# Kernel tuning notes

Hardware: AMD Instinct MI355X
Metric: run time of the kernel (lower is better)

The kernel has to match this reference:

```python
import jax, jax.numpy as jnp
import numpy as np


def setup_inputs() -> dict:
    key = jax.random.key(0)
    ks = jax.random.split(key, 8)
    B, N, A, H = 2, 2048, 256, 8
    KD = A // H  # key_dim per head = 32
    VD = A // H  # value_dim per head = 32
    return {
        "q_data": jax.random.normal(ks[0], (B, N, A), dtype=jnp.float32),
        "bias": jax.random.normal(ks[1], (B, N), dtype=jnp.float32),
        "nonbatched_bias": jax.random.normal(ks[2], (H, N, N), dtype=jnp.float32),
        "query_w": jax.random.normal(ks[3], (A, H, KD), dtype=jnp.float32) * 0.05,
        "query_b": jax.random.normal(ks[4], (1, H, KD), dtype=jnp.float32) * 0.05,
        "key_w": jax.random.normal(ks[5], (A, H, KD), dtype=jnp.float32) * 0.05,
        "value_w": jax.random.normal(ks[6], (A, H, VD), dtype=jnp.float32) * 0.05,
        "gating_w": jax.random.normal(ks[7], (A, H, VD), dtype=jnp.float32) * 0.05,
    }


def reference(q_data, bias, nonbatched_bias, query_w, query_b, key_w, value_w, gating_w):
    # q_data: [b, n, a]; bias: [b, n_k]; nonbatched_bias: [h, n_q, n_k]
    key_dim = query_w.shape[-1]
    scale = key_dim ** (-0.5)
    # projections (fused QKV in the original kernel)
    q = (jnp.einsum("bqa,ahc->bqhc", q_data, query_w) + query_b) * scale  # [b,q,h,c]
    k = jnp.einsum("bka,ahc->bkhc", q_data, key_w)                        # [b,k,h,c]
    v = jnp.einsum("bka,ahv->bkhv", q_data, value_w)                      # [b,k,h,v]
    # attention logits + batched bias (over keys) + shared nonbatched bias
    logits = jnp.einsum("bqhc,bkhc->bhqk", q, k)
    logits = logits + bias[:, None, None, :] + nonbatched_bias[None]
    weights = jax.nn.softmax(logits, axis=-1)                             # [b,h,q,k]
    weighted = jnp.einsum("bhqk,bkhv->bqhv", weights, v)                  # [b,q,h,v]
    # sigmoid gating branch fused after value projection
    gate = jax.nn.sigmoid(jnp.einsum("bqa,ahv->bqhv", q_data, gating_w))
    return weighted * gate                                                # [b,q,h,v]
```

## Files before the change

kernel.cpp:

```cpp
#include <hip/hip_runtime.h>
#include <stdint.h>

#define NTOK 2048
#define SCALE 0.17677669529663687f

typedef short s16x8 __attribute__((ext_vector_type(8)));
typedef unsigned short u16x8 __attribute__((ext_vector_type(8)));
typedef float f32x4 __attribute__((ext_vector_type(4)));

__device__ __forceinline__ unsigned short f2bf(float f) {
  unsigned int u = __builtin_bit_cast(unsigned int, f);
  u += 0x7fffu + ((u >> 16) & 1u);
  return (unsigned short)(u >> 16);
}

__global__ __launch_bounds__(256) void prep_weights_k(
    const float* __restrict__ qw, const float* __restrict__ kw,
    const float* __restrict__ vw, const float* __restrict__ gw,
    unsigned short* __restrict__ Wt) {
  __shared__ float tile[64][68];
  const int p = blockIdx.z;
  const int a0 = blockIdx.x * 64;
  const int n0 = blockIdx.y * 64;
  const float* src = (p == 0) ? qw : (p == 1) ? kw : (p == 2) ? vw : gw;
  const int tx = threadIdx.x & 15;
  const int ty = threadIdx.x >> 4;
#pragma unroll
  for (int kk = 0; kk < 4; kk++) {
    int ar = ty + kk * 16;
    float4 v = *reinterpret_cast<const float4*>(src + (a0 + ar) * 256 + n0 + tx * 4);
    tile[ar][tx * 4 + 0] = v.x; tile[ar][tx * 4 + 1] = v.y;
    tile[ar][tx * 4 + 2] = v.z; tile[ar][tx * 4 + 3] = v.w;
  }
  __syncthreads();
  unsigned short* dst = Wt + p * 65536;
#pragma unroll
  for (int kk = 0; kk < 4; kk++) {
    int nr = ty + kk * 16;
    ushort4 o;
    o.x = f2bf(tile[tx * 4 + 0][nr]);
    o.y = f2bf(tile[tx * 4 + 1][nr]);
    o.z = f2bf(tile[tx * 4 + 2][nr]);
    o.w = f2bf(tile[tx * 4 + 3][nr]);
    *reinterpret_cast<ushort4*>(dst + (n0 + nr) * 256 + a0 + tx * 4) = o;
  }
}

__global__ __launch_bounds__(256) void proj_k(
    const float* __restrict__ x, const unsigned short* __restrict__ Wt,
    const float* __restrict__ query_b,
    unsigned short* __restrict__ Qg, unsigned short* __restrict__ Kg,
    unsigned short* __restrict__ Vt, float* __restrict__ gate) {
  const int w = threadIdx.x >> 6;
  const int lane = threadIdx.x & 63;
  const int l15 = lane & 15;
  const int quad = lane >> 4;
  const int p = blockIdx.y >> 1;
  const int half = blockIdx.y & 1;
  const int rbase = blockIdx.x * 128 + w * 32;
  const unsigned short* wp = Wt + p * 65536;

  f32x4 acc[2][8];
#pragma unroll
  for (int rt = 0; rt < 2; rt++)
#pragma unroll
    for (int ct = 0; ct < 8; ct++) acc[rt][ct] = (f32x4){0.f, 0.f, 0.f, 0.f};

  for (int ks = 0; ks < 8; ks++) {
    const int kb = ks * 32;
    s16x8 af[2];
#pragma unroll
    for (int rt = 0; rt < 2; rt++) {
      const float* xr = x + (rbase + rt * 16 + l15) * 256 + kb + quad * 8;
      float4 f0 = *reinterpret_cast<const float4*>(xr);
      float4 f1 = *reinterpret_cast<const float4*>(xr + 4);
      u16x8 t;
      t[0] = f2bf(f0.x); t[1] = f2bf(f0.y); t[2] = f2bf(f0.z); t[3] = f2bf(f0.w);
      t[4] = f2bf(f1.x); t[5] = f2bf(f1.y); t[6] = f2bf(f1.z); t[7] = f2bf(f1.w);
      af[rt] = __builtin_bit_cast(s16x8, t);
    }
#pragma unroll
    for (int ct = 0; ct < 8; ct++) {
      uint4 bv = *reinterpret_cast<const uint4*>(
          wp + (half * 128 + ct * 16 + l15) * 256 + kb + quad * 8);
      s16x8 bfr = __builtin_bit_cast(s16x8, bv);
#pragma unroll
      for (int rt = 0; rt < 2; rt++)
        acc[rt][ct] = __builtin_amdgcn_mfma_f32_16x16x32_bf16(af[rt], bfr, acc[rt][ct], 0, 0, 0);
    }
  }

#pragma unroll
  for (int ct = 0; ct < 8; ct++) {
    const int cgl = half * 128 + ct * 16 + l15;
    const int h = cgl >> 5, c = cgl & 31;
#pragma unroll
    for (int rt = 0; rt < 2; rt++) {
      const int n0r = rbase + rt * 16 + quad * 4;
      const int bidx = n0r >> 11;
      const int nl0 = n0r & 2047;
      if (p == 0) {
        const float qb = query_b[cgl];
#pragma unroll
        for (int i = 0; i < 4; i++) {
          float v = (acc[rt][ct][i] + qb) * SCALE;
          Qg[(size_t)((bidx * 8 + h) * 2048 + nl0 + i) * 32 + c] = f2bf(v);
        }
      } else if (p == 1) {
#pragma unroll
        for (int i = 0; i < 4; i++)
          Kg[(size_t)((bidx * 8 + h) * 2048 + nl0 + i) * 32 + c] = f2bf(acc[rt][ct][i]);
      } else if (p == 2) {
        ushort4 o;
        o.x = f2bf(acc[rt][ct][0]); o.y = f2bf(acc[rt][ct][1]);
        o.z = f2bf(acc[rt][ct][2]); o.w = f2bf(acc[rt][ct][3]);
        *reinterpret_cast<ushort4*>(Vt + (size_t)((bidx * 8 + h) * 32 + c) * 2048 + nl0) = o;
      } else {
#pragma unroll
        for (int i = 0; i < 4; i++) {
          float s = 1.f / (1.f + __expf(-acc[rt][ct][i]));
          gate[(size_t)(bidx * 2048 + nl0 + i) * 256 + cgl] = s;
        }
      }
    }
  }
}

#define PST 136
__global__ __launch_bounds__(128, 2) void attn_k(
    const unsigned short* __restrict__ Qg, const unsigned short* __restrict__ Kg,
    const unsigned short* __restrict__ Vt, const float* __restrict__ bias,
    const float* __restrict__ nb, const float* __restrict__ gate,
    float* __restrict__ out) {
  __shared__ unsigned short Ps[2 * 16 * PST];
  const int w = threadIdx.x >> 6;
  const int lane = threadIdx.x & 63;
  const int l15 = lane & 15;
  const int quad = lane >> 4;
  const int h = blockIdx.y, b = blockIdx.z;
  const int bh = b * 8 + h;
  const int qbase = blockIdx.x * 32 + w * 16;
  const unsigned short* Qp = Qg + (size_t)bh * 2048 * 32;
  const unsigned short* Kp = Kg + (size_t)bh * 2048 * 32;
  const unsigned short* Vp = Vt + (size_t)bh * 32 * 2048;
  const float* nbp = nb + (size_t)h * 2048 * 2048;
  const float* biasp = bias + b * 2048;
  unsigned short* Pw = Ps + w * 16 * PST;

  s16x8 aq = __builtin_bit_cast(s16x8, *reinterpret_cast<const uint4*>(
      Qp + (size_t)(qbase + l15) * 32 + quad * 8));
  const int qr0 = qbase + quad * 4;

  float mst[4], lst[4];
  f32x4 o[2];
#pragma unroll
  for (int i = 0; i < 4; i++) { mst[i] = -INFINITY; lst[i] = 0.f; }
#pragma unroll
  for (int vt = 0; vt < 2; vt++) o[vt] = (f32x4){0.f, 0.f, 0.f, 0.f};

  float nbuf[2][32];
  float bb[2][8];
#pragma unroll
  for (int ct = 0; ct < 8; ct++) {
    bb[0][ct] = biasp[ct * 16 + l15];
#pragma unroll
    for (int i = 0; i < 4; i++)
      nbuf[0][ct * 4 + i] = nbp[(size_t)(qr0 + i) * 2048 + ct * 16 + l15];
  }

#pragma unroll 2
  for (int kt = 0; kt < 16; kt++) {
    const int kb = kt * 128;
    const int cur = kt & 1, nxt = cur ^ 1;

    s16x8 bk[8];
#pragma unroll
    for (int ct = 0; ct < 8; ct++)
      bk[ct] = __builtin_bit_cast(s16x8, *reinterpret_cast<const uint4*>(
          Kp + (size_t)(kb + ct * 16 + l15) * 32 + quad * 8));

    if (kt < 15) {
      const int kb2 = kb + 128;
#pragma unroll
      for (int ct = 0; ct < 8; ct++) {
        bb[nxt][ct] = biasp[kb2 + ct * 16 + l15];
#pragma unroll
        for (int i = 0; i < 4; i++)
          nbuf[nxt][ct * 4 + i] = nbp[(size_t)(qr0 + i) * 2048 + kb2 + ct * 16 + l15];
      }
    }

    f32x4 s[8];
#pragma unroll
    for (int ct = 0; ct < 8; ct++)
      s[ct] = __builtin_amdgcn_mfma_f32_16x16x32_bf16(
          aq, bk[ct], (f32x4){0.f, 0.f, 0.f, 0.f}, 0, 0, 0);

    s16x8 vbf[4][2];
#pragma unroll
    for (int kc = 0; kc < 4; kc++)
#pragma unroll
      for (int vt = 0; vt < 2; vt++)
        vbf[kc][vt] = __builtin_bit_cast(s16x8, *reinterpret_cast<const uint4*>(
            Vp + (size_t)(vt * 16 + l15) * 2048 + kb + kc * 32 + quad * 8));

#pragma unroll
    for (int ct = 0; ct < 8; ct++)
#pragma unroll
      for (int i = 0; i < 4; i++) s[ct][i] += bb[cur][ct] + nbuf[cur][ct * 4 + i];

    float alpha[4];
#pragma unroll
    for (int i = 0; i < 4; i++) {
      float mx = s[0][i];
#pragma unroll
      for (int ct = 1; ct < 8; ct++) mx = fmaxf(mx, s[ct][i]);
      mx = fmaxf(mx, __shfl_xor(mx, 1));
      mx = fmaxf(mx, __shfl_xor(mx, 2));
      mx = fmaxf(mx, __shfl_xor(mx, 4));
      mx = fmaxf(mx, __shfl_xor(mx, 8));
      float mn = fmaxf(mst[i], mx);
      alpha[i] = __expf(mst[i] - mn);
      mst[i] = mn;
      float sum = 0.f;
#pragma unroll
      for (int ct = 0; ct < 8; ct++) {
        float pv = __expf(s[ct][i] - mn);
        Pw[(quad * 4 + i) * PST + ct * 16 + l15] = f2bf(pv);
        sum += pv;
      }
      sum += __shfl_xor(sum, 1);
      sum += __shfl_xor(sum, 2);
      sum += __shfl_xor(sum, 4);
      sum += __shfl_xor(sum, 8);
      lst[i] = lst[i] * alpha[i] + sum;
    }
#pragma unroll
    for (int vt = 0; vt < 2; vt++)
#pragma unroll
      for (int i = 0; i < 4; i++) o[vt][i] *= alpha[i];

#pragma unroll
    for (int kc = 0; kc < 4; kc++) {
      s16x8 ap = __builtin_bit_cast(s16x8, *reinterpret_cast<const uint4*>(
          &Pw[l15 * PST + kc * 32 + quad * 8]));
#pragma unroll
      for (int vt = 0; vt < 2; vt++)
        o[vt] = __builtin_amdgcn_mfma_f32_16x16x32_bf16(ap, vbf[kc][vt], o[vt], 0, 0, 0);
    }
  }

#pragma unroll
  for (int vt = 0; vt < 2; vt++)
#pragma unroll
    for (int i = 0; i < 4; i++) {
      const int q = qr0 + i;
      const int v = vt * 16 + l15;
      const size_t oidx = (size_t)(b * 2048 + q) * 256 + h * 32 + v;
      out[oidx] = (o[vt][i] / lst[i]) * gate[oidx];
    }
}

extern "C" void kernel_launch(void* const* d_in, const int* in_sizes, int n_in,
                              void* d_out, int out_size, void* d_ws, size_t ws_size,
                              hipStream_t stream) {
  const float* q_data = (const float*)d_in[0];
  const float* bias = (const float*)d_in[1];
  const float* nbb = (const float*)d_in[2];
  const float* qw = (const float*)d_in[3];
  const float* qb = (const float*)d_in[4];
  const float* kw = (const float*)d_in[5];
  const float* vw = (const float*)d_in[6];
  const float* gw = (const float*)d_in[7];
  float* out = (float*)d_out;

  char* ws = (char*)d_ws;
  unsigned short* Wt = (unsigned short*)(ws + 0);
  unsigned short* Qg = (unsigned short*)(ws + 524288);
  unsigned short* Kg = (unsigned short*)(ws + 2621440);
  unsigned short* Vt = (unsigned short*)(ws + 4718592);
  float* gate = (float*)(ws + 6815744);

  prep_weights_k<<<dim3(4, 4, 4), 256, 0, stream>>>(qw, kw, vw, gw, Wt);
  proj_k<<<dim3(32, 8), 256, 0, stream>>>(q_data, Wt, qb, Qg, Kg, Vt, gate);
  attn_k<<<dim3(64, 8, 2), 128, 0, stream>>>(Qg, Kg, Vt, bias, nbb, gate, out);
}
```

Before: 258.0 us.

## Share nonbatched bias tile across both batches via async global-to-LDS loads

The attention kernel now covers both batch elements in one 256-thread block, so the nonbatched bias tile (which depends only on head, not batch) is read from global memory once and shared through LDS. The tile is double-buffered with asynchronous global_load_lds transfers, using an XOR swizzle to avoid bank conflicts, and a block barrier is added each iteration. This halves global traffic for the largest input but adds LDS reads, a per-iteration __syncthreads, and coupling between batch waves.

```diff
diff --git a/kernel.cpp b/kernel.cpp
--- a/kernel.cpp
+++ b/kernel.cpp
@@ -12,6 +12,12 @@
   unsigned int u = __builtin_bit_cast(unsigned int, f);
   u += 0x7fffu + ((u >> 16) & 1u);
   return (unsigned short)(u >> 16);
+}
+
+__device__ __forceinline__ void gld_lds16(const float* g, float* l) {
+  __builtin_amdgcn_global_load_lds(
+      (const __attribute__((address_space(1))) unsigned int*)g,
+      (__attribute__((address_space(3))) unsigned int*)l, 16, 0, 0);
 }
 
 __global__ __launch_bounds__(256) void prep_weights_k(
@@ -127,25 +133,41 @@
 }
 
 #define PST 136
-__global__ __launch_bounds__(128, 2) void attn_k(
+__global__ __launch_bounds__(256, 2) void attn_k(
     const unsigned short* __restrict__ Qg, const unsigned short* __restrict__ Kg,
     const unsigned short* __restrict__ Vt, const float* __restrict__ bias,
     const float* __restrict__ nb, const float* __restrict__ gate,
     float* __restrict__ out) {
-  __shared__ unsigned short Ps[2 * 16 * PST];
+  __shared__ float NbS[2][32 * 128];
+  __shared__ unsigned short Ps[4 * 16 * PST];
   const int w = threadIdx.x >> 6;
   const int lane = threadIdx.x & 63;
   const int l15 = lane & 15;
   const int quad = lane >> 4;
-  const int h = blockIdx.y, b = blockIdx.z;
+  const int qsub = w >> 1;
+  const int b = w & 1;
+  const int h = blockIdx.y;
   const int bh = b * 8 + h;
-  const int qbase = blockIdx.x * 32 + w * 16;
+  const int qtile = blockIdx.x * 32;
+  const int qbase = qtile + qsub * 16;
   const unsigned short* Qp = Qg + (size_t)bh * 2048 * 32;
   const unsigned short* Kp = Kg + (size_t)bh * 2048 * 32;
   const unsigned short* Vp = Vt + (size_t)bh * 32 * 2048;
-  const float* nbp = nb + (size_t)h * 2048 * 2048;
   const float* biasp = bias + b * 2048;
   unsigned short* Pw = Ps + w * 16 * PST;
+
+  const float* nbt = nb + (size_t)h * 2048 * 2048 + (size_t)qtile * 2048;
+  const float* nbl[4];
+  {
+    const int rsub = lane >> 5;
+    const int cblk = lane & 31;
+#pragma unroll
+    for (int j = 0; j < 4; j++) {
+      const int r = w * 8 + j * 2 + rsub;
+      const int c = (cblk ^ (r & 7)) * 4;
+      nbl[j] = nbt + (size_t)r * 2048 + c;
+    }
+  }
 
   s16x8 aq = __builtin_bit_cast(s16x8, *reinterpret_cast<const uint4*>(
       Qp + (size_t)(qbase + l15) * 32 + quad * 8));
@@ -158,15 +180,13 @@
 #pragma unroll
   for (int vt = 0; vt < 2; vt++) o[vt] = (f32x4){0.f, 0.f, 0.f, 0.f};
 
-  float nbuf[2][32];
   float bb[2][8];
 #pragma unroll
-  for (int ct = 0; ct < 8; ct++) {
-    bb[0][ct] = biasp[ct * 16 + l15];
-#pragma unroll
-    for (int i = 0; i < 4; i++)
-      nbuf[0][ct * 4 + i] = nbp[(size_t)(qr0 + i) * 2048 + ct * 16 + l15];
-  }
+  for (int ct = 0; ct < 8; ct++) bb[0][ct] = biasp[ct * 16 + l15];
+
+#pragma unroll
+  for (int j = 0; j < 4; j++) gld_lds16(nbl[j], &NbS[0][(w * 8 + j * 2) * 128]);
+  __syncthreads();
 
 #pragma unroll 2
   for (int kt = 0; kt < 16; kt++) {
@@ -179,15 +199,23 @@
       bk[ct] = __builtin_bit_cast(s16x8, *reinterpret_cast<const uint4*>(
           Kp + (size_t)(kb + ct * 16 + l15) * 32 + quad * 8));
 
+    s16x8 vbf[4][2];
+#pragma unroll
+    for (int kc = 0; kc < 4; kc++)
+#pragma unroll
+      for (int vt = 0; vt < 2; vt++)
+        vbf[kc][vt] = __builtin_bit_cast(s16x8, *reinterpret_cast<const uint4*>(
+            Vp + (size_t)(vt * 16 + l15) * 2048 + kb + kc * 32 + quad * 8));
+
     if (kt < 15) {
       const int kb2 = kb + 128;
 #pragma unroll
-      for (int ct = 0; ct < 8; ct++) {
-        bb[nxt][ct] = biasp[kb2 + ct * 16 + l15];
-#pragma unroll
-        for (int i = 0; i < 4; i++)
-          nbuf[nxt][ct * 4 + i] = nbp[(size_t)(qr0 + i) * 2048 + kb2 + ct * 16 + l15];
-      }
+      for (int ct = 0; ct < 8; ct++) bb[nxt][ct] = biasp[kb2 + ct * 16 + l15];
+      __builtin_amdgcn_sched_barrier(0);
+#pragma unroll
+      for (int j = 0; j < 4; j++)
+        gld_lds16(nbl[j] + kb2, &NbS[nxt][(w * 8 + j * 2) * 128]);
+      __builtin_amdgcn_sched_barrier(0);
     }
 
     f32x4 s[8];
@@ -196,18 +224,16 @@
       s[ct] = __builtin_amdgcn_mfma_f32_16x16x32_bf16(
           aq, bk[ct], (f32x4){0.f, 0.f, 0.f, 0.f}, 0, 0, 0);
 
-    s16x8 vbf[4][2];
-#pragma unroll
-    for (int kc = 0; kc < 4; kc++)
-#pragma unroll
-      for (int vt = 0; vt < 2; vt++)
-        vbf[kc][vt] = __builtin_bit_cast(s16x8, *reinterpret_cast<const uint4*>(
-            Vp + (size_t)(vt * 16 + l15) * 2048 + kb + kc * 32 + quad * 8));
-
-#pragma unroll
-    for (int ct = 0; ct < 8; ct++)
-#pragma unroll
-      for (int i = 0; i < 4; i++) s[ct][i] += bb[cur][ct] + nbuf[cur][ct * 4 + i];
+#pragma unroll
+    for (int i = 0; i < 4; i++) {
+      const int rsw = (quad * 4 + i) & 7;
+      const int rbase = (qsub * 16 + quad * 4 + i) * 128;
+#pragma unroll
+      for (int ct = 0; ct < 8; ct++) {
+        const int col = ct * 16 + l15;
+        s[ct][i] += bb[cur][ct] + NbS[cur][rbase + (col ^ (rsw * 4))];
+      }
+    }
 
     float alpha[4];
 #pragma unroll
@@ -248,6 +274,8 @@
       for (int vt = 0; vt < 2; vt++)
         o[vt] = __builtin_amdgcn_mfma_f32_16x16x32_bf16(ap, vbf[kc][vt], o[vt], 0, 0, 0);
     }
+
+    __syncthreads();
   }
 
 #pragma unroll
@@ -283,5 +311,5 @@
 
   prep_weights_k<<<dim3(4, 4, 4), 256, 0, stream>>>(qw, kw, vw, gw, Wt);
   proj_k<<<dim3(32, 8), 256, 0, stream>>>(q_data, Wt, qb, Qg, Kg, Vt, gate);
-  attn_k<<<dim3(64, 8, 2), 128, 0, stream>>>(Qg, Kg, Vt, bias, nbb, gate, out);
-}
+  attn_k<<<dim3(64, 8), 256, 0, stream>>>(Qg, Kg, Vt, bias, nbb, gate, out);
+}
```

After: 258.3 us. No clear change (+0.1%).

## Split attention key range across two blocks and merge partials in combine kernel

Applied to the files above, without the earlier changes.

Splits the key dimension of the attention kernel into two halves, each handled by its own block, which doubles the grid so more blocks are in flight. Each block writes unnormalized partial outputs plus running max and sum, and a new combine kernel merges the two halves with log-sum-exp rescaling and applies the gate. It also raises the occupancy hint in launch bounds, moves the V loads earlier, and fences the bias prefetch with scheduling barriers. The cost is an extra kernel launch and an extra round trip of partial results through global memory.

```diff
diff --git a/kernel.cpp b/kernel.cpp
--- a/kernel.cpp
+++ b/kernel.cpp
@@ -127,19 +127,22 @@
 }
 
 #define PST 136
-__global__ __launch_bounds__(128, 2) void attn_k(
+__global__ __launch_bounds__(128, 4) void attn_k(
     const unsigned short* __restrict__ Qg, const unsigned short* __restrict__ Kg,
     const unsigned short* __restrict__ Vt, const float* __restrict__ bias,
-    const float* __restrict__ nb, const float* __restrict__ gate,
-    float* __restrict__ out) {
+    const float* __restrict__ nb,
+    float* __restrict__ po, float* __restrict__ pm, float* __restrict__ pl) {
   __shared__ unsigned short Ps[2 * 16 * PST];
   const int w = threadIdx.x >> 6;
   const int lane = threadIdx.x & 63;
   const int l15 = lane & 15;
   const int quad = lane >> 4;
-  const int h = blockIdx.y, b = blockIdx.z;
+  const int h = blockIdx.y;
+  const int b = blockIdx.z >> 1;
+  const int sp = blockIdx.z & 1;
   const int bh = b * 8 + h;
   const int qbase = blockIdx.x * 32 + w * 16;
+  const int kt0 = sp * 8;
   const unsigned short* Qp = Qg + (size_t)bh * 2048 * 32;
   const unsigned short* Kp = Kg + (size_t)bh * 2048 * 32;
   const unsigned short* Vp = Vt + (size_t)bh * 32 * 2048;
@@ -162,14 +165,14 @@
   float bb[2][8];
 #pragma unroll
   for (int ct = 0; ct < 8; ct++) {
-    bb[0][ct] = biasp[ct * 16 + l15];
+    bb[0][ct] = biasp[kt0 * 128 + ct * 16 + l15];
 #pragma unroll
     for (int i = 0; i < 4; i++)
-      nbuf[0][ct * 4 + i] = nbp[(size_t)(qr0 + i) * 2048 + ct * 16 + l15];
+      nbuf[0][ct * 4 + i] = nbp[(size_t)(qr0 + i) * 2048 + kt0 * 128 + ct * 16 + l15];
   }
 
 #pragma unroll 2
-  for (int kt = 0; kt < 16; kt++) {
+  for (int kt = kt0; kt < kt0 + 8; kt++) {
     const int kb = kt * 128;
     const int cur = kt & 1, nxt = cur ^ 1;
 
@@ -179,8 +182,17 @@
       bk[ct] = __builtin_bit_cast(s16x8, *reinterpret_cast<const uint4*>(
           Kp + (size_t)(kb + ct * 16 + l15) * 32 + quad * 8));
 
-    if (kt < 15) {
+    s16x8 vbf[4][2];
+#pragma unroll
+    for (int kc = 0; kc < 4; kc++)
+#pragma unroll
+      for (int vt = 0; vt < 2; vt++)
+        vbf[kc][vt] = __builtin_bit_cast(s16x8, *reinterpret_cast<const uint4*>(
+            Vp + (size_t)(vt * 16 + l15) * 2048 + kb + kc * 32 + quad * 8));
+
+    if (kt < kt0 + 7) {
       const int kb2 = kb + 128;
+      __builtin_amdgcn_sched_barrier(0);
 #pragma unroll
       for (int ct = 0; ct < 8; ct++) {
         bb[nxt][ct] = biasp[kb2 + ct * 16 + l15];
@@ -188,6 +200,7 @@
         for (int i = 0; i < 4; i++)
           nbuf[nxt][ct * 4 + i] = nbp[(size_t)(qr0 + i) * 2048 + kb2 + ct * 16 + l15];
       }
+      __builtin_amdgcn_sched_barrier(0);
     }
 
     f32x4 s[8];
@@ -195,14 +208,6 @@
     for (int ct = 0; ct < 8; ct++)
       s[ct] = __builtin_amdgcn_mfma_f32_16x16x32_bf16(
           aq, bk[ct], (f32x4){0.f, 0.f, 0.f, 0.f}, 0, 0, 0);
-
-    s16x8 vbf[4][2];
-#pragma unroll
-    for (int kc = 0; kc < 4; kc++)
-#pragma unroll
-      for (int vt = 0; vt < 2; vt++)
-        vbf[kc][vt] = __builtin_bit_cast(s16x8, *reinterpret_cast<const uint4*>(
-            Vp + (size_t)(vt * 16 + l15) * 2048 + kb + kc * 32 + quad * 8));
 
 #pragma unroll
     for (int ct = 0; ct < 8; ct++)
@@ -250,15 +255,41 @@
     }
   }
 
+  const size_t pbase = (size_t)(sp * 16 + bh) * 2048;
 #pragma unroll
   for (int vt = 0; vt < 2; vt++)
 #pragma unroll
     for (int i = 0; i < 4; i++) {
       const int q = qr0 + i;
-      const int v = vt * 16 + l15;
-      const size_t oidx = (size_t)(b * 2048 + q) * 256 + h * 32 + v;
-      out[oidx] = (o[vt][i] / lst[i]) * gate[oidx];
-    }
+      po[(pbase + q) * 32 + vt * 16 + l15] = o[vt][i];
+    }
+  if (l15 == 0) {
+#pragma unroll
+    for (int i = 0; i < 4; i++) {
+      pm[pbase + qr0 + i] = mst[i];
+      pl[pbase + qr0 + i] = lst[i];
+    }
+  }
+}
+
+__global__ __launch_bounds__(256) void combine_k(
+    const float* __restrict__ po, const float* __restrict__ pm,
+    const float* __restrict__ pl, const float* __restrict__ gate,
+    float* __restrict__ out) {
+  const int bq = blockIdx.x;
+  const int b = bq >> 11, q = bq & 2047;
+  const int h = threadIdx.x >> 5, v = threadIdx.x & 31;
+  const int bh = b * 8 + h;
+  const size_t i0 = (size_t)(0 * 16 + bh) * 2048 + q;
+  const size_t i1 = (size_t)(1 * 16 + bh) * 2048 + q;
+  const float m0 = pm[i0], m1 = pm[i1];
+  const float l0 = pl[i0], l1 = pl[i1];
+  const float M = fmaxf(m0, m1);
+  const float a0 = __expf(m0 - M), a1 = __expf(m1 - M);
+  const float l = l0 * a0 + l1 * a1;
+  const float ov = po[i0 * 32 + v] * a0 + po[i1 * 32 + v] * a1;
+  const size_t oidx = (size_t)(b * 2048 + q) * 256 + h * 32 + v;
+  out[oidx] = (ov / l) * gate[oidx];
 }
 
 extern "C" void kernel_launch(void* const* d_in, const int* in_sizes, int n_in,
@@ -280,8 +311,12 @@
   unsigned short* Kg = (unsigned short*)(ws + 2621440);
   unsigned short* Vt = (unsigned short*)(ws + 4718592);
   float* gate = (float*)(ws + 6815744);
+  float* po = (float*)(ws + 11010048);
+  float* pm = (float*)(ws + 19398656);
+  float* pl = (float*)(ws + 19660800);
 
   prep_weights_k<<<dim3(4, 4, 4), 256, 0, stream>>>(qw, kw, vw, gw, Wt);
   proj_k<<<dim3(32, 8), 256, 0, stream>>>(q_data, Wt, qb, Qg, Kg, Vt, gate);
-  attn_k<<<dim3(64, 8, 2), 128, 0, stream>>>(Qg, Kg, Vt, bias, nbb, gate, out);
-}
+  attn_k<<<dim3(64, 8, 4), 128, 0, stream>>>(Qg, Kg, Vt, bias, nbb, po, pm, pl);
+  combine_k<<<dim3(4096), 256, 0, stream>>>(po, pm, pl, gate, out);
+}
```

New measurement: 589.8 us. 2.29x slower.
